# Kernel optimization log

Hardware: AMD Instinct MI355X
Metric: run time of the kernel (lower is better)

## Reference

```python
import jax, jax.numpy as jnp
import numpy as np

K = 3      # kernel size
P = 1      # padding
HEADS = 6  # num_heads


def setup_inputs() -> dict:
    key = jax.random.key(0)
    ks = jax.random.split(key, 6)
    B, H, W, C = 2, 48, 48, 192
    kk4h = K ** 4 * HEADS  # 486
    sc = 0.02
    return {
        "x": jax.random.normal(ks[0], (B, H, W, C), jnp.float32),
        "v_w": jax.random.normal(ks[1], (C, C), jnp.float32) * sc,
        "attn_w": jax.random.normal(ks[2], (kk4h, C), jnp.float32) * sc,
        "attn_b": jax.random.normal(ks[3], (kk4h,), jnp.float32) * sc,
        "proj_w": jax.random.normal(ks[4], (C, C), jnp.float32) * sc,
        "proj_b": jax.random.normal(ks[5], (C,), jnp.float32) * sc,
    }


def reference(x, v_w, attn_w, attn_b, proj_w, proj_b):
    # OutlookAttention with k=3, s=1 (pool is identity, h=H, w=W), p=1
    B, H, W, C = x.shape
    hd = C // HEADS
    scale = float(hd) ** -0.5

    # value projection (Linear, no bias): [B,H,W,C]
    v = x @ v_w.T

    # unfold: gather kxk neighborhood per pixel, row-major kernel order
    vp = jnp.pad(v, ((0, 0), (P, P), (P, P), (0, 0)))
    patches = jnp.stack(
        [vp[:, ki:ki + H, kj:kj + W, :] for ki in range(K) for kj in range(K)],
        axis=3,
    )  # [B,H,W,k*k,C]
    # -> [B, heads, hw, k*k, hd]
    v_ = patches.reshape(B, H * W, K * K, HEADS, hd).transpose(0, 3, 1, 2, 4)

    # attention logits from (pooled == identity) x: [B,H,W,k^4*heads]
    a = x @ attn_w.T + attn_b
    a = a.reshape(B, H * W, HEADS, K * K, K * K).transpose(0, 2, 1, 3, 4)
    a = jax.nn.softmax(a * scale, axis=-1)  # [B,heads,hw,kk,kk]

    # windowed attention
    out = jnp.einsum("bnlij,bnljd->bnlid", a, v_)  # [B,heads,hw,kk,hd]

    # fold (col2im): scatter-add each kernel tap back, then crop padding
    o = out.transpose(0, 2, 3, 1, 4).reshape(B, H, W, K * K, C)
    acc = jnp.zeros((B, H + 2 * P, W + 2 * P, C), dtype=o.dtype)
    idx = 0
    for ki in range(K):
        for kj in range(K):
            acc = acc.at[:, ki:ki + H, kj:kj + W, :].add(o[:, :, :, idx, :])
            idx += 1
    folded = acc[:, P:P + H, P:P + W, :]

    return folded @ proj_w.T + proj_b
```

## Files before the change

### kernel.cpp

```cpp
#include <hip/hip_runtime.h>

#define BB 2
#define HH 48
#define WW 48
#define CC 192
#define NHEADS 6
#define HD 32
#define KK 9
#define FF 486
#define NPIX (BB*HH*WW)
#define SCALE 0.17677669529663687f

typedef __bf16 bf16;
typedef __attribute__((ext_vector_type(4))) __bf16 bf16x4;
typedef __attribute__((ext_vector_type(8))) __bf16 bf16x8;
typedef __attribute__((ext_vector_type(4))) float f32x4;

#define BM 128
#define BN 64
#define KD 192
#define LDA 200

__device__ __forceinline__ void gemm_core(
    const float* __restrict__ X, const float* __restrict__ W,
    const float* __restrict__ bias, float* __restrict__ OUT,
    int m0, int n0, int Ndim,
    bf16 (*As)[LDA], bf16 (*Bs)[LDA])
{
    const int tid = threadIdx.x;

    #pragma unroll
    for (int i = 0; i < 24; ++i) {
        const int f = tid + i * 256;
        const int row = f / 48, colf = f % 48;
        const float4 xv = *(const float4*)(X + (size_t)(m0 + row) * KD + colf * 4);
        bf16x4 t = { (__bf16)xv.x, (__bf16)xv.y, (__bf16)xv.z, (__bf16)xv.w };
        *(bf16x4*)(&As[row][colf * 4]) = t;
    }
    #pragma unroll
    for (int i = 0; i < 12; ++i) {
        const int f = tid + i * 256;
        const int row = f / 48, colf = f % 48;
        float4 wv = make_float4(0.f, 0.f, 0.f, 0.f);
        if (n0 + row < Ndim)
            wv = *(const float4*)(W + (size_t)(n0 + row) * KD + colf * 4);
        bf16x4 t = { (__bf16)wv.x, (__bf16)wv.y, (__bf16)wv.z, (__bf16)wv.w };
        *(bf16x4*)(&Bs[row][colf * 4]) = t;
    }
    __syncthreads();

    const int wave = tid >> 6, lane = tid & 63;
    const int wm = (wave >> 1) * 64;
    const int wn = (wave & 1) * 32;
    const int lrow = lane & 15;
    const int lk   = (lane >> 4) * 8;

    f32x4 acc[4][2] = {};
    #pragma unroll
    for (int ks = 0; ks < 6; ++ks) {
        bf16x8 bfr[2];
        #pragma unroll
        for (int j = 0; j < 2; ++j)
            bfr[j] = *(const bf16x8*)(&Bs[wn + j * 16 + lrow][ks * 32 + lk]);
        #pragma unroll
        for (int i = 0; i < 4; ++i) {
            bf16x8 afr = *(const bf16x8*)(&As[wm + i * 16 + lrow][ks * 32 + lk]);
            #pragma unroll
            for (int j = 0; j < 2; ++j)
                acc[i][j] = __builtin_amdgcn_mfma_f32_16x16x32_bf16(afr, bfr[j], acc[i][j], 0, 0, 0);
        }
    }

    const int crow = (lane >> 4) * 4;
    #pragma unroll
    for (int j = 0; j < 2; ++j) {
        const int col = n0 + wn + j * 16 + lrow;
        if (col < Ndim) {
            const float bv = bias ? bias[col] : 0.f;
            #pragma unroll
            for (int i = 0; i < 4; ++i) {
                #pragma unroll
                for (int r = 0; r < 4; ++r) {
                    const int row = m0 + wm + i * 16 + crow + r;
                    OUT[(size_t)row * Ndim + col] = acc[i][j][r] + bv;
                }
            }
        }
    }
}

__global__ __launch_bounds__(256) void gemm_va_kernel(
    const float* __restrict__ x, const float* __restrict__ vw,
    const float* __restrict__ aw, const float* __restrict__ ab,
    float* __restrict__ v, float* __restrict__ a)
{
    __shared__ bf16 As[BM][LDA];
    __shared__ bf16 Bs[BN][LDA];
    const int m0 = blockIdx.x * BM;
    const int by = blockIdx.y;
    if (by < 3) gemm_core(x, vw, nullptr, v, m0, by * 64, CC, As, Bs);
    else        gemm_core(x, aw, ab,      a, m0, (by - 3) * 64, FF, As, Bs);
}

__global__ __launch_bounds__(256) void gemm_proj_kernel(
    const float* __restrict__ folded, const float* __restrict__ pw,
    const float* __restrict__ pb, float* __restrict__ out)
{
    __shared__ bf16 As[BM][LDA];
    __shared__ bf16 Bs[BN][LDA];
    gemm_core(folded, pw, pb, out, blockIdx.x * BM, blockIdx.y * 64, CC, As, Bs);
}

__global__ void attn_kernel(const float* __restrict__ v, const float* __restrict__ a,
                            float* __restrict__ o) {
    int n = blockIdx.x;
    int tid = threadIdx.x;
    int b = n / (HH * WW), rem = n % (HH * WW), h = rem / WW, w = rem % WW;
    __shared__ float p[FF];
    __shared__ float vl[KK][CC];

    for (int f = tid; f < FF; f += CC) p[f] = a[n * FF + f];
    #pragma unroll
    for (int j = 0; j < KK; ++j) {
        int hh = h + j / 3 - 1, ww = w + j % 3 - 1;
        if (hh >= 0 && hh < HH && ww >= 0 && ww < WW)
            vl[j][tid] = v[((b * HH + hh) * WW + ww) * CC + tid];
        else
            vl[j][tid] = 0.f;
    }
    __syncthreads();

    if (tid < NHEADS * KK) {
        float* row = p + tid * KK;
        float t[KK];
        float m = -1e30f;
        #pragma unroll
        for (int j = 0; j < KK; ++j) { t[j] = row[j] * SCALE; m = fmaxf(m, t[j]); }
        float s = 0.f;
        #pragma unroll
        for (int j = 0; j < KK; ++j) { t[j] = __expf(t[j] - m); s += t[j]; }
        float inv = 1.f / s;
        #pragma unroll
        for (int j = 0; j < KK; ++j) row[j] = t[j] * inv;
    }
    __syncthreads();

    int head = tid / HD;
    const float* ph = p + head * 81;
    #pragma unroll
    for (int i = 0; i < KK; ++i) {
        float acc = 0.f;
        #pragma unroll
        for (int j = 0; j < KK; ++j) acc += ph[i * 9 + j] * vl[j][tid];
        o[(n * KK + i) * CC + tid] = acc;
    }
}

__global__ void fold_kernel(const float* __restrict__ o, float* __restrict__ folded) {
    int idx = blockIdx.x * blockDim.x + threadIdx.x;
    if (idx >= NPIX * CC) return;
    int c = idx % CC, n = idx / CC;
    int b = n / (HH * WW), rem = n % (HH * WW), y = rem / WW, x = rem % WW;
    float s = 0.f;
    #pragma unroll
    for (int ki = 0; ki < 3; ++ki) {
        #pragma unroll
        for (int kj = 0; kj < 3; ++kj) {
            int hh = y + 1 - ki, ww = x + 1 - kj;
            if (hh >= 0 && hh < HH && ww >= 0 && ww < WW)
                s += o[(((b * HH + hh) * WW + ww) * KK + (ki * 3 + kj)) * CC + c];
        }
    }
    folded[idx] = s;
}

extern "C" void kernel_launch(void* const* d_in, const int* in_sizes, int n_in,
                              void* d_out, int out_size, void* d_ws, size_t ws_size,
                              hipStream_t stream) {
    const float* x   = (const float*)d_in[0];
    const float* vw  = (const float*)d_in[1];
    const float* aw  = (const float*)d_in[2];
    const float* ab  = (const float*)d_in[3];
    const float* pw  = (const float*)d_in[4];
    const float* pb  = (const float*)d_in[5];
    float* out = (float*)d_out;

    float* v      = (float*)d_ws;
    float* a      = v + (size_t)NPIX * CC;
    float* o      = a + (size_t)NPIX * FF;
    float* folded = o + (size_t)NPIX * KK * CC;

    dim3 blk(256);
    dim3 grid_va(NPIX / BM, 3 + 8);
    dim3 grid_pj(NPIX / BM, CC / BN);

    gemm_va_kernel<<<grid_va, blk, 0, stream>>>(x, vw, aw, ab, v, a);
    attn_kernel<<<NPIX, CC, 0, stream>>>(v, a, o);
    fold_kernel<<<(NPIX * CC) / 256, 256, 0, stream>>>(o, folded);
    gemm_proj_kernel<<<grid_pj, blk, 0, stream>>>(folded, pw, pb, out);
}
```

Measured before the change: 111.5 us.

## Tile attention over 8-pixel rows and fuse fold into projection GEMM

The attention kernel now handles 8 adjacent pixels per 256-thread block and loads a shared 3x10 halo of value vectors once with float4 loads, so neighbouring pixels no longer each re-read their 9 value rows. The separate fold kernel and its intermediate buffer are removed. The fold's 9-tap gather-sum now happens inside the A-tile load of a smaller 64x64 projection GEMM tile. This cuts one launch and a full write and read of the folded tensor. The cost is that the o tensor is gathered redundantly by the three GEMM column blocks.

```diff
diff --git a/kernel.cpp b/kernel.cpp
--- a/kernel.cpp
+++ b/kernel.cpp
@@ -102,76 +102,149 @@
     else        gemm_core(x, aw, ab,      a, m0, (by - 3) * 64, FF, As, Bs);
 }
 
-__global__ __launch_bounds__(256) void gemm_proj_kernel(
-    const float* __restrict__ folded, const float* __restrict__ pw,
+__global__ __launch_bounds__(256) void attn8_kernel(
+    const float* __restrict__ v, const float* __restrict__ a,
+    float* __restrict__ o)
+{
+    const int blk = blockIdx.x;
+    const int t = threadIdx.x;
+    const int bx = blk % 6;
+    const int rem = blk / 6;
+    const int y = rem % HH, b = rem / HH;
+    const int x0 = bx * 8;
+
+    __shared__ float vl[3][10][CC];
+    __shared__ float pa[8][FF];
+
+    for (int i = t; i < 30 * 48; i += 256) {
+        const int pos = i / 48, c4 = i % 48;
+        const int ry = pos / 10, rx = pos % 10;
+        const int gy = y + ry - 1, gx = x0 + rx - 1;
+        float4 val = make_float4(0.f, 0.f, 0.f, 0.f);
+        if (gy >= 0 && gy < HH && gx >= 0 && gx < WW)
+            val = *(const float4*)(v + ((size_t)(b * HH + gy) * WW + gx) * CC + c4 * 4);
+        *(float4*)(&vl[ry][rx][c4 * 4]) = val;
+    }
+    const int nbase = (b * HH + y) * WW + x0;
+    for (int i = t; i < 8 * 243; i += 256) {
+        const int px = i / 243, c2 = i % 243;
+        *(float2*)(&pa[px][c2 * 2]) = *(const float2*)(a + (size_t)(nbase + px) * FF + c2 * 2);
+    }
+    __syncthreads();
+
+    for (int r = t; r < 432; r += 256) {
+        const int px = r / 54, hr = r % 54;
+        float* row = &pa[px][hr * 9];
+        float tv[KK];
+        float m = -1e30f;
+        #pragma unroll
+        for (int j = 0; j < KK; ++j) { tv[j] = row[j] * SCALE; m = fmaxf(m, tv[j]); }
+        float s = 0.f;
+        #pragma unroll
+        for (int j = 0; j < KK; ++j) { tv[j] = __expf(tv[j] - m); s += tv[j]; }
+        const float inv = 1.f / s;
+        #pragma unroll
+        for (int j = 0; j < KK; ++j) row[j] = tv[j] * inv;
+    }
+    __syncthreads();
+
+    for (int px = 0; px < 8; ++px) {
+        float* ob = o + (size_t)(nbase + px) * KK * CC;
+        #pragma unroll
+        for (int r = 0; r < 7; ++r) {
+            const int idx = r * 256 + t;
+            if (idx < KK * CC) {
+                const int i = idx / CC, c = idx % CC;
+                const float* ph = &pa[px][(c / HD) * 81 + i * 9];
+                float acc = 0.f;
+                #pragma unroll
+                for (int j = 0; j < KK; ++j)
+                    acc += ph[j] * vl[j / 3][px + j % 3][c];
+                ob[idx] = acc;
+            }
+        }
+    }
+}
+
+__global__ __launch_bounds__(256) void proj_fold_kernel(
+    const float* __restrict__ o, const float* __restrict__ pw,
     const float* __restrict__ pb, float* __restrict__ out)
 {
-    __shared__ bf16 As[BM][LDA];
-    __shared__ bf16 Bs[BN][LDA];
-    gemm_core(folded, pw, pb, out, blockIdx.x * BM, blockIdx.y * 64, CC, As, Bs);
-}
-
-__global__ void attn_kernel(const float* __restrict__ v, const float* __restrict__ a,
-                            float* __restrict__ o) {
-    int n = blockIdx.x;
-    int tid = threadIdx.x;
-    int b = n / (HH * WW), rem = n % (HH * WW), h = rem / WW, w = rem % WW;
-    __shared__ float p[FF];
-    __shared__ float vl[KK][CC];
-
-    for (int f = tid; f < FF; f += CC) p[f] = a[n * FF + f];
-    #pragma unroll
-    for (int j = 0; j < KK; ++j) {
-        int hh = h + j / 3 - 1, ww = w + j % 3 - 1;
-        if (hh >= 0 && hh < HH && ww >= 0 && ww < WW)
-            vl[j][tid] = v[((b * HH + hh) * WW + ww) * CC + tid];
-        else
-            vl[j][tid] = 0.f;
-    }
-    __syncthreads();
-
-    if (tid < NHEADS * KK) {
-        float* row = p + tid * KK;
-        float t[KK];
-        float m = -1e30f;
-        #pragma unroll
-        for (int j = 0; j < KK; ++j) { t[j] = row[j] * SCALE; m = fmaxf(m, t[j]); }
-        float s = 0.f;
-        #pragma unroll
-        for (int j = 0; j < KK; ++j) { t[j] = __expf(t[j] - m); s += t[j]; }
-        float inv = 1.f / s;
-        #pragma unroll
-        for (int j = 0; j < KK; ++j) row[j] = t[j] * inv;
-    }
-    __syncthreads();
-
-    int head = tid / HD;
-    const float* ph = p + head * 81;
-    #pragma unroll
-    for (int i = 0; i < KK; ++i) {
-        float acc = 0.f;
-        #pragma unroll
-        for (int j = 0; j < KK; ++j) acc += ph[i * 9 + j] * vl[j][tid];
-        o[(n * KK + i) * CC + tid] = acc;
-    }
-}
-
-__global__ void fold_kernel(const float* __restrict__ o, float* __restrict__ folded) {
-    int idx = blockIdx.x * blockDim.x + threadIdx.x;
-    if (idx >= NPIX * CC) return;
-    int c = idx % CC, n = idx / CC;
-    int b = n / (HH * WW), rem = n % (HH * WW), y = rem / WW, x = rem % WW;
-    float s = 0.f;
-    #pragma unroll
-    for (int ki = 0; ki < 3; ++ki) {
-        #pragma unroll
-        for (int kj = 0; kj < 3; ++kj) {
-            int hh = y + 1 - ki, ww = x + 1 - kj;
-            if (hh >= 0 && hh < HH && ww >= 0 && ww < WW)
-                s += o[(((b * HH + hh) * WW + ww) * KK + (ki * 3 + kj)) * CC + c];
-        }
-    }
-    folded[idx] = s;
+    __shared__ bf16 As[64][LDA];
+    __shared__ bf16 Bs[64][LDA];
+    const int t = threadIdx.x;
+    const int m0 = blockIdx.x * 64;
+    const int n0 = blockIdx.y * 64;
+
+    #pragma unroll
+    for (int i = 0; i < 12; ++i) {
+        const int f = t + i * 256;
+        const int row = f / 48, c4 = f % 48;
+        const int n = m0 + row;
+        const int b = n / (HH * WW), r2 = n % (HH * WW), y = r2 / WW, x = r2 % WW;
+        float4 s = make_float4(0.f, 0.f, 0.f, 0.f);
+        #pragma unroll
+        for (int ki = 0; ki < 3; ++ki) {
+            const int gy = y + 1 - ki;
+            if (gy < 0 || gy >= HH) continue;
+            #pragma unroll
+            for (int kj = 0; kj < 3; ++kj) {
+                const int gx = x + 1 - kj;
+                if (gx < 0 || gx >= WW) continue;
+                const float4 ov = *(const float4*)(
+                    o + (((size_t)(b * HH + gy) * WW + gx) * KK + ki * 3 + kj) * CC + c4 * 4);
+                s.x += ov.x; s.y += ov.y; s.z += ov.z; s.w += ov.w;
+            }
+        }
+        bf16x4 tv = { (__bf16)s.x, (__bf16)s.y, (__bf16)s.z, (__bf16)s.w };
+        *(bf16x4*)(&As[row][c4 * 4]) = tv;
+    }
+    #pragma unroll
+    for (int i = 0; i < 12; ++i) {
+        const int f = t + i * 256;
+        const int row = f / 48, c4 = f % 48;
+        const float4 wv = *(const float4*)(pw + (size_t)(n0 + row) * KD + c4 * 4);
+        bf16x4 tv = { (__bf16)wv.x, (__bf16)wv.y, (__bf16)wv.z, (__bf16)wv.w };
+        *(bf16x4*)(&Bs[row][c4 * 4]) = tv;
+    }
+    __syncthreads();
+
+    const int wave = t >> 6, lane = t & 63;
+    const int wm = (wave >> 1) * 32;
+    const int wn = (wave & 1) * 32;
+    const int lrow = lane & 15;
+    const int lk   = (lane >> 4) * 8;
+
+    f32x4 acc[2][2] = {};
+    #pragma unroll
+    for (int ks = 0; ks < 6; ++ks) {
+        bf16x8 afr[2], bfr[2];
+        #pragma unroll
+        for (int j = 0; j < 2; ++j) {
+            afr[j] = *(const bf16x8*)(&As[wm + j * 16 + lrow][ks * 32 + lk]);
+            bfr[j] = *(const bf16x8*)(&Bs[wn + j * 16 + lrow][ks * 32 + lk]);
+        }
+        #pragma unroll
+        for (int i = 0; i < 2; ++i)
+            #pragma unroll
+            for (int j = 0; j < 2; ++j)
+                acc[i][j] = __builtin_amdgcn_mfma_f32_16x16x32_bf16(afr[i], bfr[j], acc[i][j], 0, 0, 0);
+    }
+
+    const int crow = (lane >> 4) * 4;
+    #pragma unroll
+    for (int j = 0; j < 2; ++j) {
+        const int col = n0 + wn + j * 16 + lrow;
+        const float bv = pb[col];
+        #pragma unroll
+        for (int i = 0; i < 2; ++i) {
+            #pragma unroll
+            for (int r = 0; r < 4; ++r) {
+                const int row = m0 + wm + i * 16 + crow + r;
+                out[(size_t)row * CC + col] = acc[i][j][r] + bv;
+            }
+        }
+    }
 }
 
 extern "C" void kernel_launch(void* const* d_in, const int* in_sizes, int n_in,
@@ -185,17 +258,15 @@
     const float* pb  = (const float*)d_in[5];
     float* out = (float*)d_out;
 
-    float* v      = (float*)d_ws;
-    float* a      = v + (size_t)NPIX * CC;
-    float* o      = a + (size_t)NPIX * FF;
-    float* folded = o + (size_t)NPIX * KK * CC;
+    float* v = (float*)d_ws;
+    float* a = v + (size_t)NPIX * CC;
+    float* o = a + (size_t)NPIX * FF;
 
     dim3 blk(256);
     dim3 grid_va(NPIX / BM, 3 + 8);
-    dim3 grid_pj(NPIX / BM, CC / BN);
+    dim3 grid_pj(NPIX / 64, CC / 64);
 
     gemm_va_kernel<<<grid_va, blk, 0, stream>>>(x, vw, aw, ab, v, a);
-    attn_kernel<<<NPIX, CC, 0, stream>>>(v, a, o);
-    fold_kernel<<<(NPIX * CC) / 256, 256, 0, stream>>>(o, folded);
-    gemm_proj_kernel<<<grid_pj, blk, 0, stream>>>(folded, pw, pb, out);
-}
+    attn8_kernel<<<2 * HH * (WW / 8), blk, 0, stream>>>(v, a, o);
+    proj_fold_kernel<<<grid_pj, blk, 0, stream>>>(o, pw, pb, out);
+}
```

Result: slower. 138.9 us (+24.6%).

## Fuse fold into projection GEMM and shrink GEMM tiles for more blocks

Applied to the files above, without the earlier changes.

The separate fold kernel is removed. The projection GEMM now gathers and sums the 9 kernel-tap contributions from the attention output while loading its A tile, which avoids writing and re-reading the folded buffer and saves one launch. The V/attn GEMM tile shrinks from 128 to 64 rows and the projection uses 32-row tiles, so the grids have more blocks to fill the GPU. The cost is that each projection block re-reads the o tensor for all 3 N-tiles, tripling o traffic, and the small tiles reuse the weights less.

```diff
diff --git a/kernel.cpp b/kernel.cpp
--- a/kernel.cpp
+++ b/kernel.cpp
@@ -16,59 +16,65 @@
 typedef __attribute__((ext_vector_type(8))) __bf16 bf16x8;
 typedef __attribute__((ext_vector_type(4))) float f32x4;
 
-#define BM 128
-#define BN 64
 #define KD 192
 #define LDA 200
 
-__device__ __forceinline__ void gemm_core(
-    const float* __restrict__ X, const float* __restrict__ W,
-    const float* __restrict__ bias, float* __restrict__ OUT,
-    int m0, int n0, int Ndim,
-    bf16 (*As)[LDA], bf16 (*Bs)[LDA])
+__global__ __launch_bounds__(256) void gemm_va_kernel(
+    const float* __restrict__ x, const float* __restrict__ vw,
+    const float* __restrict__ aw, const float* __restrict__ ab,
+    float* __restrict__ v, float* __restrict__ a)
 {
-    const int tid = threadIdx.x;
-
-    #pragma unroll
-    for (int i = 0; i < 24; ++i) {
-        const int f = tid + i * 256;
-        const int row = f / 48, colf = f % 48;
-        const float4 xv = *(const float4*)(X + (size_t)(m0 + row) * KD + colf * 4);
-        bf16x4 t = { (__bf16)xv.x, (__bf16)xv.y, (__bf16)xv.z, (__bf16)xv.w };
-        *(bf16x4*)(&As[row][colf * 4]) = t;
-    }
+    __shared__ bf16 As[64][LDA];
+    __shared__ bf16 Bs[64][LDA];
+    const int t = threadIdx.x;
+    const int m0 = blockIdx.x * 64;
+    const int by = blockIdx.y;
+    const bool is_v = (by < 3);
+    const int n0 = is_v ? by * 64 : (by - 3) * 64;
+    const int Ndim = is_v ? CC : FF;
+    const float* W = is_v ? vw : aw;
+    float* OUT = is_v ? v : a;
+
     #pragma unroll
     for (int i = 0; i < 12; ++i) {
-        const int f = tid + i * 256;
-        const int row = f / 48, colf = f % 48;
+        const int f = t + i * 256;
+        const int row = f / 48, c4 = f % 48;
+        const float4 xv = *(const float4*)(x + (size_t)(m0 + row) * KD + c4 * 4);
+        bf16x4 tv = { (__bf16)xv.x, (__bf16)xv.y, (__bf16)xv.z, (__bf16)xv.w };
+        *(bf16x4*)(&As[row][c4 * 4]) = tv;
+    }
+    #pragma unroll
+    for (int i = 0; i < 12; ++i) {
+        const int f = t + i * 256;
+        const int row = f / 48, c4 = f % 48;
         float4 wv = make_float4(0.f, 0.f, 0.f, 0.f);
         if (n0 + row < Ndim)
-            wv = *(const float4*)(W + (size_t)(n0 + row) * KD + colf * 4);
-        bf16x4 t = { (__bf16)wv.x, (__bf16)wv.y, (__bf16)wv.z, (__bf16)wv.w };
-        *(bf16x4*)(&Bs[row][colf * 4]) = t;
-    }
-    __syncthreads();
-
-    const int wave = tid >> 6, lane = tid & 63;
-    const int wm = (wave >> 1) * 64;
+            wv = *(const float4*)(W + (size_t)(n0 + row) * KD + c4 * 4);
+        bf16x4 tv = { (__bf16)wv.x, (__bf16)wv.y, (__bf16)wv.z, (__bf16)wv.w };
+        *(bf16x4*)(&Bs[row][c4 * 4]) = tv;
+    }
+    __syncthreads();
+
+    const int wave = t >> 6, lane = t & 63;
+    const int wm = (wave >> 1) * 32;
     const int wn = (wave & 1) * 32;
     const int lrow = lane & 15;
     const int lk   = (lane >> 4) * 8;
 
-    f32x4 acc[4][2] = {};
+    f32x4 acc[2][2] = {};
     #pragma unroll
     for (int ks = 0; ks < 6; ++ks) {
-        bf16x8 bfr[2];
-        #pragma unroll
-        for (int j = 0; j < 2; ++j)
+        bf16x8 afr[2], bfr[2];
+        #pragma unroll
+        for (int j = 0; j < 2; ++j) {
+            afr[j] = *(const bf16x8*)(&As[wm + j * 16 + lrow][ks * 32 + lk]);
             bfr[j] = *(const bf16x8*)(&Bs[wn + j * 16 + lrow][ks * 32 + lk]);
-        #pragma unroll
-        for (int i = 0; i < 4; ++i) {
-            bf16x8 afr = *(const bf16x8*)(&As[wm + i * 16 + lrow][ks * 32 + lk]);
+        }
+        #pragma unroll
+        for (int i = 0; i < 2; ++i)
             #pragma unroll
             for (int j = 0; j < 2; ++j)
-                acc[i][j] = __builtin_amdgcn_mfma_f32_16x16x32_bf16(afr, bfr[j], acc[i][j], 0, 0, 0);
-        }
+                acc[i][j] = __builtin_amdgcn_mfma_f32_16x16x32_bf16(afr[i], bfr[j], acc[i][j], 0, 0, 0);
     }
 
     const int crow = (lane >> 4) * 4;
@@ -76,9 +82,9 @@
     for (int j = 0; j < 2; ++j) {
         const int col = n0 + wn + j * 16 + lrow;
         if (col < Ndim) {
-            const float bv = bias ? bias[col] : 0.f;
+            const float bv = is_v ? 0.f : ab[col];
             #pragma unroll
-            for (int i = 0; i < 4; ++i) {
+            for (int i = 0; i < 2; ++i) {
                 #pragma unroll
                 for (int r = 0; r < 4; ++r) {
                     const int row = m0 + wm + i * 16 + crow + r;
@@ -87,28 +93,6 @@
             }
         }
     }
-}
-
-__global__ __launch_bounds__(256) void gemm_va_kernel(
-    const float* __restrict__ x, const float* __restrict__ vw,
-    const float* __restrict__ aw, const float* __restrict__ ab,
-    float* __restrict__ v, float* __restrict__ a)
-{
-    __shared__ bf16 As[BM][LDA];
-    __shared__ bf16 Bs[BN][LDA];
-    const int m0 = blockIdx.x * BM;
-    const int by = blockIdx.y;
-    if (by < 3) gemm_core(x, vw, nullptr, v, m0, by * 64, CC, As, Bs);
-    else        gemm_core(x, aw, ab,      a, m0, (by - 3) * 64, FF, As, Bs);
-}
-
-__global__ __launch_bounds__(256) void gemm_proj_kernel(
-    const float* __restrict__ folded, const float* __restrict__ pw,
-    const float* __restrict__ pb, float* __restrict__ out)
-{
-    __shared__ bf16 As[BM][LDA];
-    __shared__ bf16 Bs[BN][LDA];
-    gemm_core(folded, pw, pb, out, blockIdx.x * BM, blockIdx.y * 64, CC, As, Bs);
 }
 
 __global__ void attn_kernel(const float* __restrict__ v, const float* __restrict__ a,
@@ -156,22 +140,74 @@
     }
 }
 
-__global__ void fold_kernel(const float* __restrict__ o, float* __restrict__ folded) {
-    int idx = blockIdx.x * blockDim.x + threadIdx.x;
-    if (idx >= NPIX * CC) return;
-    int c = idx % CC, n = idx / CC;
-    int b = n / (HH * WW), rem = n % (HH * WW), y = rem / WW, x = rem % WW;
-    float s = 0.f;
-    #pragma unroll
-    for (int ki = 0; ki < 3; ++ki) {
-        #pragma unroll
-        for (int kj = 0; kj < 3; ++kj) {
-            int hh = y + 1 - ki, ww = x + 1 - kj;
-            if (hh >= 0 && hh < HH && ww >= 0 && ww < WW)
-                s += o[(((b * HH + hh) * WW + ww) * KK + (ki * 3 + kj)) * CC + c];
-        }
-    }
-    folded[idx] = s;
+__global__ __launch_bounds__(256) void proj_fold_kernel(
+    const float* __restrict__ o, const float* __restrict__ pw,
+    const float* __restrict__ pb, float* __restrict__ out)
+{
+    __shared__ bf16 As[32][LDA];
+    __shared__ bf16 Bs[64][LDA];
+    const int t = threadIdx.x;
+    const int m0 = blockIdx.x * 32;
+    const int n0 = blockIdx.y * 64;
+
+    for (int i = 0; i < 6; ++i) {
+        const int f = t + i * 256;
+        const int row = f / 48, c4 = f % 48;
+        const int n = m0 + row;
+        const int b = n / (HH * WW), r2 = n % (HH * WW), y = r2 / WW, x = r2 % WW;
+        float4 s = make_float4(0.f, 0.f, 0.f, 0.f);
+        for (int ki = 0; ki < 3; ++ki) {
+            const int gy = y + 1 - ki;
+            if (gy < 0 || gy >= HH) continue;
+            for (int kj = 0; kj < 3; ++kj) {
+                const int gx = x + 1 - kj;
+                if (gx < 0 || gx >= WW) continue;
+                const float4 ov = *(const float4*)(
+                    o + (((size_t)(b * HH + gy) * WW + gx) * KK + ki * 3 + kj) * CC + c4 * 4);
+                s.x += ov.x; s.y += ov.y; s.z += ov.z; s.w += ov.w;
+            }
+        }
+        bf16x4 tv = { (__bf16)s.x, (__bf16)s.y, (__bf16)s.z, (__bf16)s.w };
+        *(bf16x4*)(&As[row][c4 * 4]) = tv;
+    }
+    #pragma unroll
+    for (int i = 0; i < 12; ++i) {
+        const int f = t + i * 256;
+        const int row = f / 48, c4 = f % 48;
+        const float4 wv = *(const float4*)(pw + (size_t)(n0 + row) * KD + c4 * 4);
+        bf16x4 tv = { (__bf16)wv.x, (__bf16)wv.y, (__bf16)wv.z, (__bf16)wv.w };
+        *(bf16x4*)(&Bs[row][c4 * 4]) = tv;
+    }
+    __syncthreads();
+
+    const int wave = t >> 6, lane = t & 63;
+    const int wm = (wave & 1) * 16;
+    const int wn = (wave >> 1) * 32;
+    const int lrow = lane & 15;
+    const int lk   = (lane >> 4) * 8;
+
+    f32x4 acc[2] = {};
+    #pragma unroll
+    for (int ks = 0; ks < 6; ++ks) {
+        bf16x8 afr = *(const bf16x8*)(&As[wm + lrow][ks * 32 + lk]);
+        #pragma unroll
+        for (int j = 0; j < 2; ++j) {
+            bf16x8 bfr = *(const bf16x8*)(&Bs[wn + j * 16 + lrow][ks * 32 + lk]);
+            acc[j] = __builtin_amdgcn_mfma_f32_16x16x32_bf16(afr, bfr, acc[j], 0, 0, 0);
+        }
+    }
+
+    const int crow = (lane >> 4) * 4;
+    #pragma unroll
+    for (int j = 0; j < 2; ++j) {
+        const int col = n0 + wn + j * 16 + lrow;
+        const float bv = pb[col];
+        #pragma unroll
+        for (int r = 0; r < 4; ++r) {
+            const int row = m0 + wm + crow + r;
+            out[(size_t)row * CC + col] = acc[j][r] + bv;
+        }
+    }
 }
 
 extern "C" void kernel_launch(void* const* d_in, const int* in_sizes, int n_in,
@@ -185,17 +221,15 @@
     const float* pb  = (const float*)d_in[5];
     float* out = (float*)d_out;
 
-    float* v      = (float*)d_ws;
-    float* a      = v + (size_t)NPIX * CC;
-    float* o      = a + (size_t)NPIX * FF;
-    float* folded = o + (size_t)NPIX * KK * CC;
+    float* v = (float*)d_ws;
+    float* a = v + (size_t)NPIX * CC;
+    float* o = a + (size_t)NPIX * FF;
 
     dim3 blk(256);
-    dim3 grid_va(NPIX / BM, 3 + 8);
-    dim3 grid_pj(NPIX / BM, CC / BN);
+    dim3 grid_va(NPIX / 64, 3 + 8);
+    dim3 grid_pj(NPIX / 32, CC / 64);
 
     gemm_va_kernel<<<grid_va, blk, 0, stream>>>(x, vw, aw, ab, v, a);
     attn_kernel<<<NPIX, CC, 0, stream>>>(v, a, o);
-    fold_kernel<<<(NPIX * CC) / 256, 256, 0, stream>>>(o, folded);
-    gemm_proj_kernel<<<grid_pj, blk, 0, stream>>>(folded, pw, pb, out);
-}
+    proj_fold_kernel<<<grid_pj, blk, 0, stream>>>(o, pw, pb, out);
+}
```

Measured after the change: 116.5 us. +4.5%, slower.
